# Optimization experiments

Hardware: AMD Instinct MI355X
Metric: run time of the kernel (lower is better)

Reference implementation:

```python
import jax, jax.numpy as jnp
import numpy as np

B, N, NG, K, H, C, BD = 4, 2048, 12, 16, 64, 128, 64
M = N // 4  # fps with down_sample=4
TWO_PI = 2.0 * np.pi


def _knn_idx(q, x, k):
    # q [Q,3] queries, x [P,3] pool -> [Q,k] indices of k nearest points in x
    d2 = jnp.sum((q[:, None, :] - x[None, :, :]) ** 2, axis=-1)
    _, idx = jax.lax.top_k(-d2, k)
    return idx


def _fps_idx(pos, m):
    # farthest point sampling, fixed m points, start at index 0
    n = pos.shape[0]
    def body(carry, _):
        d, last = carry
        dist = jnp.sum((pos - pos[last]) ** 2, axis=-1)
        d = jnp.minimum(d, dist)
        return (d, jnp.argmax(d)), last
    (_, _), idx = jax.lax.scan(body, (jnp.full((n,), 1e10, pos.dtype), jnp.int32(0)), None, length=m)
    return idx


def _basis_mlp(z, rff_w, w1, b1, w2, b2):
    # RFF -> Linear -> GELU -> Linear -> GELU
    p = TWO_PI * (z @ rff_w)
    f = jnp.concatenate([jnp.sin(p), jnp.cos(p)], axis=-1)
    h = jax.nn.gelu(f @ w1 + b1)
    return jax.nn.gelu(h @ w2 + b2)


def _interaction(x, nbr, kbx, kbR, kx_w, kx_b, kR_w, kR_b, mix_w, mix_b):
    # depthwise separable group conv: spatial gather-multiply-mean, then orientation mix
    kx = kbx @ kx_w + kx_b                     # [M,K,NG,C] spatial depthwise kernel
    kR = kbR @ kR_w + kR_b                     # [NG,NG,C] orientation depthwise kernel
    agg = jnp.mean(x[nbr] * kx, axis=1)        # [M,NG,C] mean over K neighbors
    y = jnp.einsum('bnc,mnc->bmc', agg, kR) / kR.shape[0]
    return x + jax.nn.gelu(y @ mix_w + mix_b)


def setup_inputs():
    key = jax.random.key(0)
    ks = iter(jax.random.split(key, 64))
    def randn(shape, std=1.0):
        return std * jax.random.normal(next(ks), shape, dtype=jnp.float32)
    inp = {}
    inp['pos'] = jax.random.uniform(next(ks), (B, N, 3), dtype=jnp.float32)
    nrm = randn((B, N, 3))
    inp['normal'] = nrm / jnp.linalg.norm(nrm, axis=-1, keepdims=True)
    g = randn((NG, 3))
    inp['grid'] = g / jnp.linalg.norm(g, axis=-1, keepdims=True)
    def lin(name, fin, fout):
        inp[name + '_w'] = randn((fin, fout), 1.0 / np.sqrt(fin))
        inp[name + '_b'] = jnp.zeros((fout,), jnp.float32)
    lin('emb1', 4, H); lin('emb2', H, H)
    lin('down', H, C)
    inp['bx_rff'] = randn((2, C // 2), 10.0)   # sigma=10
    lin('bx1', C, C); lin('bx2', C, BD)
    inp['bR_rff'] = randn((1, C // 2), 10.0)
    lin('bR1', C, C); lin('bR2', C, BD)
    for j in ('i1', 'i2'):
        lin(j + '_kx', BD, C); lin(j + '_kR', BD, C); lin(j + '_mix', C, C)
    lin('post1', C, 256); lin('post2', 256, 64); lin('post3', 64, 1)
    return inp


def reference(pos, normal, grid, emb1_w, emb1_b, emb2_w, emb2_b, down_w, down_b,
              bx_rff, bx1_w, bx1_b, bx2_w, bx2_b, bR_rff, bR1_w, bR1_b, bR2_w, bR2_b,
              i1_kx_w, i1_kx_b, i1_kR_w, i1_kR_b, i1_mix_w, i1_mix_b,
              i2_kx_w, i2_kx_b, i2_kR_w, i2_kR_b, i2_mix_w, i2_mix_b,
              post1_w, post1_b, post2_w, post2_b, post3_w, post3_b):
    def per_graph(p, nm):
        # lift: fiber features = <grid, normal> plus broadcast positions -> [N,NG,4]
        feat = jnp.concatenate([(nm @ grid.T)[:, :, None],
                                jnp.broadcast_to(p[:, None, :], (p.shape[0], NG, 3))], axis=-1)
        x = jax.nn.gelu(feat @ emb1_w + emb1_b) @ emb2_w + emb2_b   # [N,NG,H]
        # downsample block: fps + knn + linear/relu + scatter-max (exactly K edges per target)
        sel = _fps_idx(p, M)
        nbr_d = _knn_idx(p[sel], p, K)                               # [M,K] into N
        h = jax.nn.relu(x @ down_w + down_b)                         # [N,NG,C]
        x = jnp.max(h[nbr_d], axis=1)                                # [M,NG,C]
        ps = p[sel]
        # convolver block: knn graph + r3s2 edge attrs + basis MLPs + 2 interaction layers
        nbr = _knn_idx(ps, ps, K)                                    # [M,K] into M
        rel = ps[nbr] - ps[:, None, :]                               # pos[src]-pos[tgt], [M,K,3]
        rz = jnp.einsum('mke,ne->mkn', rel, grid)                    # [M,K,NG]
        rxy = jnp.sqrt(jnp.sum((rel[:, :, None, :] - rz[..., None] * grid) ** 2, axis=-1) + 1e-12)
        rpx = jnp.stack([rxy, rz], axis=-1)                          # [M,K,NG,2]
        rpR = (grid @ grid.T)[:, :, None]                            # [NG,NG,1]
        kbx = _basis_mlp(rpx, bx_rff, bx1_w, bx1_b, bx2_w, bx2_b)    # [M,K,NG,BD]
        kbR = _basis_mlp(rpR, bR_rff, bR1_w, bR1_b, bR2_w, bR2_b)    # [NG,NG,BD]
        x = _interaction(x, nbr, kbx, kbR, i1_kx_w, i1_kx_b, i1_kR_w, i1_kR_b, i1_mix_w, i1_mix_b)
        x = _interaction(x, nbr, kbx, kbR, i2_kx_w, i2_kx_b, i2_kR_w, i2_kR_b, i2_mix_w, i2_mix_b)
        # readout: mean over grid, global mean pool, MLP head
        g = jnp.mean(x, axis=(0, 1))                                 # [C]
        h1 = jax.nn.gelu(g @ post1_w + post1_b)
        h2 = jax.nn.gelu(h1 @ post2_w + post2_b)
        return h2 @ post3_w + post3_b                                # [1]
    return jax.vmap(per_graph)(pos, normal)                          # [B,1]
```

## Files before the change

kernel.cpp:

```cpp
#include <hip/hip_runtime.h>
#include <hip/hip_bf16.h>
#include <cfloat>

#define B_ 4
#define N_ 2048
#define NG_ 12
#define K_ 16
#define H_ 64
#define C_ 128
#define BD_ 64
#define M_ 512

typedef __attribute__((ext_vector_type(8))) short short8;
typedef __attribute__((ext_vector_type(4))) float floatx4;
typedef unsigned short ushort_t;
typedef unsigned int uint_t;

__device__ __forceinline__ float gelu_f(float x){
  float s = 0.7978845608028654f*(x + 0.044715f*x*x*x);
  float e = __expf(2.0f*s);
  float t = 1.0f - 2.0f/(e + 1.0f);
  return 0.5f*x*(1.0f + t);
}

__device__ __forceinline__ ushort_t bf16_rne(float x){
  uint_t u = __float_as_uint(x);
  uint_t r = (u + 0x7fffu + ((u >> 16) & 1u)) >> 16;
  return (ushort_t)r;
}

#define DPP_AMAX(CTRL) { \
  int _vb = __float_as_int(v); \
  int _ov = __builtin_amdgcn_update_dpp(_vb, _vb, (CTRL), 0xF, 0xF, false); \
  int _oi = __builtin_amdgcn_update_dpp(vi, vi, (CTRL), 0xF, 0xF, false); \
  float _of = __int_as_float(_ov); \
  bool _tk = (_of > v) || (_of == v && _oi < vi); \
  v = _tk ? _of : v; vi = _tk ? _oi : vi; }

#define DPP_AMIN(CTRL) { \
  int _vb = __float_as_int(v); \
  int _ov = __builtin_amdgcn_update_dpp(_vb, _vb, (CTRL), 0xF, 0xF, false); \
  int _oi = __builtin_amdgcn_update_dpp(vi, vi, (CTRL), 0xF, 0xF, false); \
  float _of = __int_as_float(_ov); \
  bool _tk = (_of < v) || (_of == v && _oi < vi); \
  v = _tk ? _of : v; vi = _tk ? _oi : vi; }

#define FPSB 4
#define LIFTB (B_*N_*NG_/4)
#define WSB 64
#define KBRB (NG_*NG_)

__global__ __launch_bounds__(256) void k_mega1(
    const float* __restrict__ pos, const float* __restrict__ normal,
    const float* __restrict__ grid,
    const float* __restrict__ e1w, const float* __restrict__ e1b,
    const float* __restrict__ e2w, const float* __restrict__ e2b,
    float* __restrict__ x1, float* __restrict__ ps,
    const float* __restrict__ bx1w, const float* __restrict__ bx2w,
    const float* __restrict__ kxw1, const float* __restrict__ kxw2,
    const float* __restrict__ dww,
    ushort_t* __restrict__ w1hiT, ushort_t* __restrict__ w1loT,
    ushort_t* __restrict__ w2hiT, ushort_t* __restrict__ w2loT,
    ushort_t* __restrict__ x1hiT, ushort_t* __restrict__ x1loT,
    ushort_t* __restrict__ x2hiT, ushort_t* __restrict__ x2loT,
    ushort_t* __restrict__ dwThi, ushort_t* __restrict__ dwTlo,
    const float* __restrict__ bR_rff,
    const float* __restrict__ bR1w, const float* __restrict__ bR1b,
    const float* __restrict__ bR2w, const float* __restrict__ bR2b,
    float* __restrict__ kbR){
  __shared__ float4 posS4[N_];
  __shared__ float2 wred[2][4];
  __shared__ float ts4[4][64];
  __shared__ float fsb[128], hsb[128];
  int bid = blockIdx.x;
  int tid = threadIdx.x;

  if (bid < FPSB){
    int b = bid;
    for (int i=tid;i<N_;i+=256){
      const float* p = pos + (size_t)b*N_*3 + (size_t)i*3;
      posS4[i] = make_float4(p[0], p[1], p[2], 0.f);
    }
    __syncthreads();
    float px[8],py[8],pz[8],d[8];
    #pragma unroll
    for (int j=0;j<8;++j){
      float4 pt = posS4[tid + 256*j];
      px[j]=pt.x; py[j]=pt.y; pz[j]=pt.z;
      d[j]=1e10f;
    }
    int wave = tid>>6, lane = tid&63;
    int last = 0;
    for (int s=0;s<M_;++s){
      float4 lp = posS4[last];
      float lx=lp.x, ly=lp.y, lz=lp.z;
      if (tid==0){ float* o = ps + ((size_t)b*M_+s)*3; o[0]=lx;o[1]=ly;o[2]=lz; }
      #pragma unroll
      for (int j=0;j<8;++j){
        float dx=__fsub_rn(px[j],lx), dy=__fsub_rn(py[j],ly), dz=__fsub_rn(pz[j],lz);
        float dist=__fadd_rn(__fadd_rn(__fmul_rn(dx,dx),__fmul_rn(dy,dy)),__fmul_rn(dz,dz));
        d[j]=fminf(d[j],dist);
      }
      if (s==M_-1) break;
      float va = d[1]>d[0]?d[1]:d[0]; int ja = d[1]>d[0]?1:0;
      float vb = d[3]>d[2]?d[3]:d[2]; int jb = d[3]>d[2]?3:2;
      float vc = d[5]>d[4]?d[5]:d[4]; int jc = d[5]>d[4]?5:4;
      float vd = d[7]>d[6]?d[7]:d[6]; int jd = d[7]>d[6]?7:6;
      float ve = vb>va?vb:va; int je = vb>va?jb:ja;
      float vf = vd>vc?vd:vc; int jf = vd>vc?jd:jc;
      float v  = vf>ve?vf:ve; int jj = vf>ve?jf:je;
      int vi = tid + (jj<<8);
      DPP_AMAX(0x121); DPP_AMAX(0x122); DPP_AMAX(0x124); DPP_AMAX(0x128);
      DPP_AMAX(0x142); DPP_AMAX(0x143);
      int sv = __builtin_amdgcn_readlane(__float_as_int(v), 63);
      int si = __builtin_amdgcn_readlane(vi, 63);
      if (lane==0) wred[s&1][wave] = make_float2(__int_as_float(sv), __int_as_float(si));
      __syncthreads();
      float2 r0 = wred[s&1][0], r1 = wred[s&1][1], r2 = wred[s&1][2], r3 = wred[s&1][3];
      float bv = r0.x; int bi = __float_as_int(r0.y);
      int i1 = __float_as_int(r1.y); if (r1.x>bv || (r1.x==bv && i1<bi)){ bv=r1.x; bi=i1; }
      int i2 = __float_as_int(r2.y); if (r2.x>bv || (r2.x==bv && i2<bi)){ bv=r2.x; bi=i2; }
      int i3 = __float_as_int(r3.y); if (r3.x>bv || (r3.x==bv && i3<bi)){ bv=r3.x; bi=i3; }
      last = bi;
    }
  } else if (bid < FPSB + LIFTB){
    int vbid = bid - FPSB;
    int q = tid>>6, lane = tid&63;
    int fid = vbid*4 + q;
    int g = fid % NG_;
    int n = (fid / NG_) % N_;
    int b = fid / (NG_*N_);
    const float* nm = normal + (size_t)(b*N_+n)*3;
    const float* pp = pos + (size_t)(b*N_+n)*3;
    const float* gg = grid + g*3;
    float f0 = nm[0]*gg[0] + nm[1]*gg[1] + nm[2]*gg[2];
    float t = e1b[lane] + f0*e1w[lane] + pp[0]*e1w[64+lane] + pp[1]*e1w[128+lane] + pp[2]*e1w[192+lane];
    ts4[q][lane] = gelu_f(t);
    __syncthreads();
    float acc = e2b[lane];
    #pragma unroll
    for (int i=0;i<64;++i) acc = fmaf(ts4[q][i], e2w[i*64+lane], acc);
    x1[(size_t)fid*64 + lane] = acc;
  } else if (bid < FPSB + LIFTB + WSB){
    int tg = (bid - FPSB - LIFTB)*256 + tid;
    if (tg < 16384){
      int j = tg >> 7, k = tg & 127;
      float x = bx1w[k*128 + j];
      ushort_t hi = bf16_rne(x);
      float hif = __uint_as_float(((uint_t)hi)<<16);
      ushort_t lo = bf16_rne(x - hif);
      w1hiT[tg] = hi; w1loT[tg] = lo;
    }
    if (tg < 8192){
      int c = tg >> 7, j = tg & 127;
      float x = bx2w[j*64 + c];
      ushort_t hi = bf16_rne(x);
      float hif = __uint_as_float(((uint_t)hi)<<16);
      ushort_t lo = bf16_rne(x - hif);
      w2hiT[tg] = hi; w2loT[tg] = lo;
    }
    if (tg < 8192){
      int c = tg >> 6, d = tg & 63;
      float xa = kxw1[d*128 + c];
      ushort_t hi = bf16_rne(xa);
      float hif = __uint_as_float(((uint_t)hi)<<16);
      ushort_t lo = bf16_rne(xa - hif);
      x1hiT[tg] = hi; x1loT[tg] = lo;
      float xb = kxw2[d*128 + c];
      ushort_t hi2 = bf16_rne(xb);
      float hif2 = __uint_as_float(((uint_t)hi2)<<16);
      ushort_t lo2 = bf16_rne(xb - hif2);
      x2hiT[tg] = hi2; x2loT[tg] = lo2;
      float xd = dww[d*128 + c];
      ushort_t hi3 = bf16_rne(xd);
      float hif3 = __uint_as_float(((uint_t)hi3)<<16);
      ushort_t lo3 = bf16_rne(xd - hif3);
      dwThi[tg] = hi3; dwTlo[tg] = lo3;
    }
  } else {
    int vbid = bid - FPSB - LIFTB - WSB;
    int gm = vbid / NG_, gn = vbid % NG_;
    int j = tid;
    if (j < 128){
      float z = grid[gm*3]*grid[gn*3] + grid[gm*3+1]*grid[gn*3+1] + grid[gm*3+2]*grid[gn*3+2];
      float ang = 6.283185307179586f * (z * bR_rff[j & 63]);
      fsb[j] = (j<64) ? sinf(ang) : cosf(ang);
    }
    __syncthreads();
    if (j < 128){
      float acc = bR1b[j];
      for (int i=0;i<128;++i) acc = fmaf(fsb[i], bR1w[i*128+j], acc);
      hsb[j] = gelu_f(acc);
    }
    __syncthreads();
    if (j < 64){
      float a2 = bR2b[j];
      for (int i=0;i<128;++i) a2 = fmaf(hsb[i], bR2w[i*64+j], a2);
      kbR[(size_t)vbid*64 + j] = gelu_f(a2);
    }
  }
}

template<int NP>
__device__ __forceinline__ void knn_body(int qm, const float* __restrict__ qp,
                                         const float* __restrict__ pool, int* __restrict__ out){
  constexpr int R = NP/64;
  int lane = threadIdx.x;
  int b = qm / M_;
  const float* q = qp + (size_t)qm*3;
  float qx=q[0], qy=q[1], qz=q[2];
  float d2[R];
  #pragma unroll
  for (int j=0;j<R;++j){
    int n = lane + 64*j;
    const float* p = pool + ((size_t)b*NP + n)*3;
    float dx=__fsub_rn(qx,p[0]), dy=__fsub_rn(qy,p[1]), dz=__fsub_rn(qz,p[2]);
    d2[j]=__fadd_rn(__fadd_rn(__fmul_rn(dx,dx),__fmul_rn(dy,dy)),__fmul_rn(dz,dz));
  }
  for (int r=0;r<K_;++r){
    float v=FLT_MAX; int vi=0x7fffffff;
    #pragma unroll
    for (int j=0;j<R;++j){
      if (d2[j]<v){ v=d2[j]; vi=lane+64*j; }
    }
    DPP_AMIN(0x121); DPP_AMIN(0x122); DPP_AMIN(0x124); DPP_AMIN(0x128);
    DPP_AMIN(0x142); DPP_AMIN(0x143);
    int si = __builtin_amdgcn_readlane(vi, 63);
    if (lane==0) out[(size_t)qm*K_ + r] = si;
    #pragma unroll
    for (int j=0;j<R;++j){ if (si == lane + 64*j) d2[j] = FLT_MAX; }
  }
}

__global__ __launch_bounds__(64) void k_knn_all(const float* __restrict__ psb,
    const float* __restrict__ pos, int* __restrict__ nbrD, int* __restrict__ nbrS){
  int bid = blockIdx.x;
  if (bid < B_*M_) knn_body<N_>(bid, psb, pos, nbrD);
  else             knn_body<M_>(bid - B_*M_, psb, psb, nbrS);
}

__global__ __launch_bounds__(128) void k_kR2(
    const float* __restrict__ kbR,
    const float* __restrict__ w1, const float* __restrict__ b1,
    const float* __restrict__ w2, const float* __restrict__ b2,
    float* __restrict__ o1, float* __restrict__ o2){
  int bid = blockIdx.x;
  int pair = bid % KBRB;
  const float* w = (bid < KBRB) ? w1 : w2;
  const float* bb = (bid < KBRB) ? b1 : b2;
  float* oo = (bid < KBRB) ? o1 : o2;
  int c = threadIdx.x;
  __shared__ float kb[64];
  if (c<64) kb[c] = kbR[(size_t)pair*64 + c];
  __syncthreads();
  float acc = bb[c];
  for (int d=0;d<64;++d) acc = fmaf(kb[d], w[d*128+c], acc);
  oo[(size_t)pair*128 + c] = acc;
}

__device__ __forceinline__ void dm_body(float* um, int bm,
    const float* __restrict__ x1, const int* __restrict__ nbrD,
    const ushort_t* __restrict__ dwThi, const ushort_t* __restrict__ dwTlo,
    const float* __restrict__ db, float* __restrict__ xA){
  int b = bm / M_;
  int tid = threadIdx.x;
  float* xs = um;
  int* nb = (int*)(um + 12288);
  if (tid < K_) nb[tid] = nbrD[(size_t)bm*K_ + tid];
  __syncthreads();
  for (int idx=tid; idx<3072; idx+=256){
    int k = idx / 192, qq = idx % 192;
    float4 vv = ((const float4*)&x1[((size_t)(b*N_) + nb[k])*(NG_*H_)])[qq];
    int gran = (qq >> 1) ^ (k & 7);
    *(float4*)&xs[k*768 + gran*8 + (qq&1)*4] = vv;
  }
  __syncthreads();
  int wid = tid>>6, lane = tid&63, ln = lane&15, g4 = lane>>4;
  short8 bh[2][2], bl[2][2];
  float dbv[2];
  #pragma unroll
  for (int nt=0; nt<2; ++nt){
    int col = wid*32 + nt*16 + ln;
    dbv[nt] = db[col];
    #pragma unroll
    for (int ks=0; ks<2; ++ks){
      bh[nt][ks] = *(const short8*)&dwThi[(size_t)col*64 + ks*32 + g4*8];
      bl[nt][ks] = *(const short8*)&dwTlo[(size_t)col*64 + ks*32 + g4*8];
    }
  }
  int xorl = ln & 7;
  #pragma unroll
  for (int g=0; g<NG_; ++g){
    short8 ah[2], al[2];
    #pragma unroll
    for (int ks=0; ks<2; ++ks){
      int col0 = g*64 + ks*32 + g4*8;
      int gran = (col0 >> 3) ^ xorl;
      const float* src = &xs[ln*768 + gran*8];
      float4 p0 = *(const float4*)src;
      float4 p1 = *(const float4*)(src+4);
      float hv[8] = {p0.x,p0.y,p0.z,p0.w,p1.x,p1.y,p1.z,p1.w};
      #pragma unroll
      for (int e=0; e<8; ++e){
        ushort_t hi = bf16_rne(hv[e]);
        float hif = __uint_as_float(((uint_t)hi)<<16);
        ushort_t lo = bf16_rne(hv[e]-hif);
        ah[ks][e] = (short)hi; al[ks][e] = (short)lo;
      }
    }
    floatx4 acc[2];
    acc[0] = (floatx4){0.f,0.f,0.f,0.f};
    acc[1] = (floatx4){0.f,0.f,0.f,0.f};
    #pragma unroll
    for (int nt=0; nt<2; ++nt)
      #pragma unroll
      for (int ks=0; ks<2; ++ks){
        acc[nt] = __builtin_amdgcn_mfma_f32_16x16x32_bf16(ah[ks], bh[nt][ks], acc[nt], 0,0,0);
        acc[nt] = __builtin_amdgcn_mfma_f32_16x16x32_bf16(al[ks], bh[nt][ks], acc[nt], 0,0,0);
        acc[nt] = __builtin_amdgcn_mfma_f32_16x16x32_bf16(ah[ks], bl[nt][ks], acc[nt], 0,0,0);
      }
    #pragma unroll
    for (int nt=0; nt<2; ++nt){
      float mx = fmaxf(fmaxf(acc[nt][0],acc[nt][1]), fmaxf(acc[nt][2],acc[nt][3]));
      mx = fmaxf(mx, __shfl_xor(mx, 16));
      mx = fmaxf(mx, __shfl_xor(mx, 32));
      if (g4 == 0)
        xA[(size_t)bm*(NG_*C_) + g*C_ + wid*32 + nt*16 + ln] = fmaxf(mx + dbv[nt], 0.0f);
    }
  }
}

__device__ __forceinline__ void kbx_body(float* um, int vbid,
    const float* __restrict__ ps, const int* __restrict__ nbr,
    const float* __restrict__ grid, const float* __restrict__ rff,
    const ushort_t* __restrict__ w1hiT, const ushort_t* __restrict__ w1loT,
    const ushort_t* __restrict__ w2hiT, const ushort_t* __restrict__ w2loT,
    const float* __restrict__ b1, const float* __restrict__ b2,
    float* __restrict__ kbx){
  float* z0s = um;
  float* z1s = um + 128;
  float* rws = um + 256;
  int tid = threadIdx.x;
  if (tid < 128){
    rws[tid] = rff[tid];
    int fid = vbid*128 + tid;
    int g = fid % NG_;
    int k = (fid/NG_) % K_;
    int bm = fid / (NG_*K_);
    int b = bm / M_;
    int nb = nbr[(size_t)bm*K_ + k];
    const float* pm = ps + (size_t)bm*3;
    const float* pn = ps + ((size_t)(b*M_) + nb)*3;
    float rx = pn[0]-pm[0], ry = pn[1]-pm[1], rz3 = pn[2]-pm[2];
    const float* gg = grid + g*3;
    float rz = rx*gg[0] + ry*gg[1] + rz3*gg[2];
    float vx = rx - rz*gg[0], vy = ry - rz*gg[1], vz = rz3 - rz*gg[2];
    float rxy = sqrtf(vx*vx + vy*vy + vz*vz + 1e-12f);
    z0s[tid]=rxy; z1s[tid]=rz;
  }
  __syncthreads();
  int wid = tid>>6, lane = tid&63;
  int ln = lane & 15, g = lane >> 4;
  float* bw = um + 384 + wid*1088;

  short8 ahi[2][4], alo[2][4];
  #pragma unroll
  for (int rt=0; rt<2; ++rt){
    float z0 = z0s[wid*32 + rt*16 + ln];
    float z1 = z1s[wid*32 + rt*16 + ln];
    #pragma unroll
    for (int ks=0; ks<4; ++ks){
      #pragma unroll
      for (int e=0; e<8; ++e){
        int kd = ks*32 + g*8 + e;
        int kk = kd & 63;
        float t = z0*rws[kk] + z1*rws[64+kk];
        t = t - floorf(t);
        float v = (ks < 2) ? __builtin_amdgcn_sinf(t) : __builtin_amdgcn_cosf(t);
        ushort_t hi = bf16_rne(v);
        float hif = __uint_as_float(((uint_t)hi)<<16);
        ushort_t lo = bf16_rne(v - hif);
        ahi[rt][ks][e] = (short)hi;
        alo[rt][ks][e] = (short)lo;
      }
    }
  }
  floatx4 acc2[2][4];
  #pragma unroll
  for (int rt=0; rt<2; ++rt)
    #pragma unroll
    for (int ct=0; ct<4; ++ct)
      acc2[rt][ct] = (floatx4){0.f,0.f,0.f,0.f};

  #pragma unroll
  for (int jp=0; jp<4; ++jp){
    floatx4 acc1[2][2];
    #pragma unroll
    for (int rt=0; rt<2; ++rt)
      #pragma unroll
      for (int jt=0; jt<2; ++jt)
        acc1[rt][jt] = (floatx4){0.f,0.f,0.f,0.f};
    #pragma unroll
    for (int ks=0; ks<4; ++ks){
      #pragma unroll
      for (int jt=0; jt<2; ++jt){
        int j = jp*32 + jt*16 + ln;
        short8 bhi = *(const short8*)&w1hiT[(size_t)j*128 + ks*32 + g*8];
        short8 blo = *(const short8*)&w1loT[(size_t)j*128 + ks*32 + g*8];
        #pragma unroll
        for (int rt=0; rt<2; ++rt){
          acc1[rt][jt] = __builtin_amdgcn_mfma_f32_16x16x32_bf16(ahi[rt][ks], bhi, acc1[rt][jt], 0,0,0);
          acc1[rt][jt] = __builtin_amdgcn_mfma_f32_16x16x32_bf16(alo[rt][ks], bhi, acc1[rt][jt], 0,0,0);
          acc1[rt][jt] = __builtin_amdgcn_mfma_f32_16x16x32_bf16(ahi[rt][ks], blo, acc1[rt][jt], 0,0,0);
        }
      }
    }
    #pragma unroll
    for (int jt=0; jt<2; ++jt){
      float bb = b1[jp*32 + jt*16 + ln];
      #pragma unroll
      for (int rt=0; rt<2; ++rt)
        #pragma unroll
        for (int i=0; i<4; ++i)
          bw[(rt*16 + g*4 + i)*34 + jt*16 + ln] = gelu_f(bb + acc1[rt][jt][i]);
    }
    #pragma unroll
    for (int rt=0; rt<2; ++rt){
      int base = (rt*16 + ln)*34 + g*8;
      float2 p0 = *(float2*)&bw[base+0];
      float2 p1 = *(float2*)&bw[base+2];
      float2 p2 = *(float2*)&bw[base+4];
      float2 p3 = *(float2*)&bw[base+6];
      float hv[8] = {p0.x,p0.y,p1.x,p1.y,p2.x,p2.y,p3.x,p3.y};
      short8 a2h, a2l;
      #pragma unroll
      for (int e=0; e<8; ++e){
        ushort_t hi = bf16_rne(hv[e]);
        float hif = __uint_as_float(((uint_t)hi)<<16);
        ushort_t lo = bf16_rne(hv[e] - hif);
        a2h[e] = (short)hi;
        a2l[e] = (short)lo;
      }
      #pragma unroll
      for (int ct=0; ct<4; ++ct){
        short8 b2h = *(const short8*)&w2hiT[(size_t)(ct*16+ln)*128 + jp*32 + g*8];
        short8 b2l = *(const short8*)&w2loT[(size_t)(ct*16+ln)*128 + jp*32 + g*8];
        acc2[rt][ct] = __builtin_amdgcn_mfma_f32_16x16x32_bf16(a2h, b2h, acc2[rt][ct], 0,0,0);
        acc2[rt][ct] = __builtin_amdgcn_mfma_f32_16x16x32_bf16(a2l, b2h, acc2[rt][ct], 0,0,0);
        acc2[rt][ct] = __builtin_amdgcn_mfma_f32_16x16x32_bf16(a2h, b2l, acc2[rt][ct], 0,0,0);
      }
    }
  }
  #pragma unroll
  for (int ct=0; ct<4; ++ct){
    float bb = b2[ct*16 + ln];
    #pragma unroll
    for (int rt=0; rt<2; ++rt)
      #pragma unroll
      for (int i=0; i<4; ++i){
        int row = wid*32 + rt*16 + g*4 + i;
        size_t fiber = (size_t)vbid*128 + row;
        kbx[fiber*64 + ct*16 + ln] = gelu_f(bb + acc2[rt][ct][i]);
      }
  }
}

__global__ __launch_bounds__(256) void k_dmkbx(
    const float* __restrict__ x1, const int* __restrict__ nbrD,
    const ushort_t* __restrict__ dwThi, const ushort_t* __restrict__ dwTlo,
    const float* __restrict__ db, float* __restrict__ xA,
    const float* __restrict__ ps, const int* __restrict__ nbrS,
    const float* __restrict__ grid, const float* __restrict__ rff,
    const ushort_t* __restrict__ w1hiT, const ushort_t* __restrict__ w1loT,
    const ushort_t* __restrict__ w2hiT, const ushort_t* __restrict__ w2loT,
    const float* __restrict__ b1, const float* __restrict__ b2,
    float* __restrict__ kbx){
  __shared__ __align__(16) float um[12384];
  int bid = blockIdx.x;
  if (bid < B_*M_)
    dm_body(um, bid, x1, nbrD, dwThi, dwTlo, db, xA);
  else
    kbx_body(um, bid - B_*M_, ps, nbrS, grid, rff, w1hiT, w1loT, w2hiT, w2loT, b1, b2, kbx);
}

__global__ __launch_bounds__(256) void k_inter(
    const float* __restrict__ xin, const int* __restrict__ nbr,
    const float* __restrict__ kbx, const float* __restrict__ kR,
    const ushort_t* __restrict__ kxhT, const ushort_t* __restrict__ kxlT,
    const float* __restrict__ kxb,
    const float* __restrict__ mw, const float* __restrict__ mb,
    float* __restrict__ xout){
  int bm = blockIdx.x; int b = bm / M_;
  int tid = threadIdx.x;
  int wid = tid>>6, lane = tid&63, ln = lane&15, g4 = lane>>4;
  int c = tid & 127, gh = tid >> 7;
  __shared__ float kbsL[48][68];
  __shared__ float Ts[48][130];
  __shared__ float aggS[NG_][C_];
  __shared__ float yS[NG_][C_];
  short8 bh[2][2], bl[2][2];
  float kxbv[2];
  #pragma unroll
  for (int nt=0; nt<2; ++nt){
    int cc_ = (wid*2+nt)*16 + ln;
    kxbv[nt] = kxb[cc_];
    #pragma unroll
    for (int ks=0; ks<2; ++ks){
      bh[nt][ks] = *(const short8*)&kxhT[(size_t)cc_*64 + ks*32 + g4*8];
      bl[nt][ks] = *(const short8*)&kxlT[(size_t)cc_*64 + ks*32 + g4*8];
    }
  }
  float accg[6] = {0,0,0,0,0,0};
  for (int cc=0; cc<4; ++cc){
    {
      const float4* src = (const float4*)(kbx + ((size_t)bm*192 + cc*48)*64);
      for (int idx=tid; idx<768; idx+=256){
        int r = idx >> 4, dq = idx & 15;
        *(float4*)&kbsL[r][dq*4] = src[idx];
      }
    }
    __syncthreads();
    floatx4 acc[3][2];
    #pragma unroll
    for (int mt=0; mt<3; ++mt)
      #pragma unroll
      for (int nt=0; nt<2; ++nt)
        acc[mt][nt] = (floatx4){0.f,0.f,0.f,0.f};
    #pragma unroll
    for (int mt=0; mt<3; ++mt){
      short8 ah[2], al[2];
      #pragma unroll
      for (int ks=0; ks<2; ++ks){
        float4 p0 = *(const float4*)&kbsL[mt*16+ln][ks*32+g4*8];
        float4 p1 = *(const float4*)&kbsL[mt*16+ln][ks*32+g4*8+4];
        float hv[8] = {p0.x,p0.y,p0.z,p0.w,p1.x,p1.y,p1.z,p1.w};
        #pragma unroll
        for (int e=0; e<8; ++e){
          ushort_t hi = bf16_rne(hv[e]);
          float hif = __uint_as_float(((uint_t)hi)<<16);
          ushort_t lo = bf16_rne(hv[e] - hif);
          ah[ks][e] = (short)hi;
          al[ks][e] = (short)lo;
        }
      }
      #pragma unroll
      for (int nt=0; nt<2; ++nt)
        #pragma unroll
        for (int ks=0; ks<2; ++ks){
          acc[mt][nt] = __builtin_amdgcn_mfma_f32_16x16x32_bf16(ah[ks], bh[nt][ks], acc[mt][nt], 0,0,0);
          acc[mt][nt] = __builtin_amdgcn_mfma_f32_16x16x32_bf16(al[ks], bh[nt][ks], acc[mt][nt], 0,0,0);
          acc[mt][nt] = __builtin_amdgcn_mfma_f32_16x16x32_bf16(ah[ks], bl[nt][ks], acc[mt][nt], 0,0,0);
        }
    }
    #pragma unroll
    for (int mt=0; mt<3; ++mt)
      #pragma unroll
      for (int nt=0; nt<2; ++nt)
        #pragma unroll
        for (int i=0; i<4; ++i)
          Ts[mt*16 + g4*4 + i][(wid*2+nt)*16 + ln] = acc[mt][nt][i] + kxbv[nt];
    __syncthreads();
    #pragma unroll
    for (int kl=0; kl<4; ++kl){
      int nb = nbr[(size_t)bm*K_ + cc*4 + kl];
      const float* xr = xin + ((size_t)(b*M_) + nb)*(NG_*C_);
      #pragma unroll
      for (int gi=0; gi<6; ++gi){
        int g = gh*6 + gi;
        accg[gi] = fmaf(Ts[kl*12+g][c], xr[g*C_ + c], accg[gi]);
      }
    }
    __syncthreads();
  }
  #pragma unroll
  for (int gi=0; gi<6; ++gi)
    aggS[gh*6+gi][c] = accg[gi] * (1.0f/16.0f);
  __syncthreads();
  #pragma unroll
  for (int gi=0; gi<6; ++gi){
    int g = gh*6+gi;
    float yv = 0.f;
    #pragma unroll
    for (int n=0;n<NG_;++n) yv = fmaf(aggS[n][c], kR[((size_t)g*NG_+n)*C_ + c], yv);
    yS[g][c] = yv * (1.0f/12.0f);
  }
  __syncthreads();
  float m6[6] = {0,0,0,0,0,0};
  for (int i4=0;i4<32;++i4){
    float w0 = mw[(i4*4+0)*C_+c], w1 = mw[(i4*4+1)*C_+c],
          w2 = mw[(i4*4+2)*C_+c], w3 = mw[(i4*4+3)*C_+c];
    #pragma unroll
    for (int gi=0;gi<6;++gi){
      int g = gh*6+gi;
      float4 yv = *(const float4*)&yS[g][i4*4];
      m6[gi] = fmaf(yv.x,w0,fmaf(yv.y,w1,fmaf(yv.z,w2,fmaf(yv.w,w3,m6[gi]))));
    }
  }
  float mbc = mb[c];
  #pragma unroll
  for (int gi=0;gi<6;++gi){
    int g = gh*6+gi;
    size_t off = (size_t)bm*(NG_*C_) + g*C_ + c;
    xout[off] = xin[off] + gelu_f(m6[gi] + mbc);
  }
}

__global__ __launch_bounds__(256) void k_reduce(
    const float* __restrict__ x, float* __restrict__ part){
  int blk = blockIdx.x;
  int b = blk >> 6, ch = blk & 63;
  int tid = threadIdx.x;
  int c = tid & 127, half = tid >> 7;
  const float* xb = x + (size_t)b*(M_*NG_)*C_;
  int r0 = ch*96;
  float acc = 0.f;
  for (int r = r0 + half; r < r0 + 96; r += 2)
    acc += xb[(size_t)r*C_ + c];
  __shared__ float red[256];
  red[tid] = acc;
  __syncthreads();
  if (half == 0)
    part[(size_t)blk*C_ + c] = red[c] + red[128 + c];
}

__global__ __launch_bounds__(256) void k_head(
    const float* __restrict__ part,
    const float* __restrict__ p1w, const float* __restrict__ p1b,
    const float* __restrict__ p2w, const float* __restrict__ p2b,
    const float* __restrict__ p3w, const float* __restrict__ p3b,
    float* __restrict__ out){
  int b = blockIdx.x, tid = threadIdx.x;
  __shared__ float gs[128];
  if (tid < 128){
    float a = 0.f;
    const float* pb = part + (size_t)b*64*C_;
    for (int ch = 0; ch < 64; ++ch) a += pb[(size_t)ch*C_ + tid];
    gs[tid] = a * (1.0f/(M_*NG_));
  }
  __syncthreads();
  __shared__ float h1[256];
  {
    float a = p1b[tid];
    for (int i=0;i<128;++i) a = fmaf(gs[i], p1w[i*256+tid], a);
    h1[tid] = gelu_f(a);
  }
  __syncthreads();
  __shared__ float h2[64];
  if (tid<64){
    float a = p2b[tid];
    for (int i=0;i<256;++i) a = fmaf(h1[i], p2w[i*64+tid], a);
    h2[tid] = gelu_f(a);
  }
  __syncthreads();
  if (tid==0){
    float a = p3b[0];
    for (int i=0;i<64;++i) a = fmaf(h2[i], p3w[i], a);
    out[b] = a;
  }
}

extern "C" void kernel_launch(void* const* d_in, const int* in_sizes, int n_in,
                              void* d_out, int out_size, void* d_ws, size_t ws_size,
                              hipStream_t stream){
  const float* pos    = (const float*)d_in[0];
  const float* normal = (const float*)d_in[1];
  const float* grid   = (const float*)d_in[2];
  const float* e1w = (const float*)d_in[3];  const float* e1b = (const float*)d_in[4];
  const float* e2w = (const float*)d_in[5];  const float* e2b = (const float*)d_in[6];
  const float* dww = (const float*)d_in[7];  const float* dwb = (const float*)d_in[8];
  const float* bx_rff = (const float*)d_in[9];
  const float* bx1w = (const float*)d_in[10]; const float* bx1b = (const float*)d_in[11];
  const float* bx2w = (const float*)d_in[12]; const float* bx2b = (const float*)d_in[13];
  const float* bR_rff = (const float*)d_in[14];
  const float* bR1w = (const float*)d_in[15]; const float* bR1b = (const float*)d_in[16];
  const float* bR2w = (const float*)d_in[17]; const float* bR2b = (const float*)d_in[18];
  const float* i1kxw = (const float*)d_in[19]; const float* i1kxb = (const float*)d_in[20];
  const float* i1kRw = (const float*)d_in[21]; const float* i1kRb = (const float*)d_in[22];
  const float* i1mw  = (const float*)d_in[23]; const float* i1mb  = (const float*)d_in[24];
  const float* i2kxw = (const float*)d_in[25]; const float* i2kxb = (const float*)d_in[26];
  const float* i2kRw = (const float*)d_in[27]; const float* i2kRb = (const float*)d_in[28];
  const float* i2mw  = (const float*)d_in[29]; const float* i2mb  = (const float*)d_in[30];
  const float* p1w = (const float*)d_in[31]; const float* p1b = (const float*)d_in[32];
  const float* p2w = (const float*)d_in[33]; const float* p2b = (const float*)d_in[34];
  const float* p3w = (const float*)d_in[35]; const float* p3b = (const float*)d_in[36];
  float* out = (float*)d_out;

  float* ws = (float*)d_ws;
  size_t o = 0;
  float* x1  = ws + o; o += (size_t)B_*N_*NG_*H_;
  float* psb = ws + o; o += (size_t)B_*M_*3;
  float* xA  = ws + o; o += (size_t)B_*M_*NG_*C_;
  float* xB  = ws + o; o += (size_t)B_*M_*NG_*C_;
  float* kbx = ws + o; o += (size_t)B_*M_*K_*NG_*BD_;
  float* kbR = ws + o; o += (size_t)NG_*NG_*BD_;
  float* kRb1 = ws + o; o += (size_t)NG_*NG_*C_;
  float* kRb2 = ws + o; o += (size_t)NG_*NG_*C_;
  float* part = ws + o; o += (size_t)B_*64*C_;
  int* nbrD  = (int*)(ws + o); o += (size_t)B_*M_*K_;
  int* nbrS  = (int*)(ws + o); o += (size_t)B_*M_*K_;
  ushort_t* w1hiT = (ushort_t*)(ws + o); o += 8192;
  ushort_t* w1loT = (ushort_t*)(ws + o); o += 8192;
  ushort_t* w2hiT = (ushort_t*)(ws + o); o += 4096;
  ushort_t* w2loT = (ushort_t*)(ws + o); o += 4096;
  ushort_t* x1hiT = (ushort_t*)(ws + o); o += 4096;
  ushort_t* x1loT = (ushort_t*)(ws + o); o += 4096;
  ushort_t* x2hiT = (ushort_t*)(ws + o); o += 4096;
  ushort_t* x2loT = (ushort_t*)(ws + o); o += 4096;
  ushort_t* dwThi = (ushort_t*)(ws + o); o += 4096;
  ushort_t* dwTlo = (ushort_t*)(ws + o); o += 4096;

  k_mega1<<<FPSB + LIFTB + WSB + KBRB, 256, 0, stream>>>(
      pos, normal, grid, e1w, e1b, e2w, e2b, x1, psb,
      bx1w, bx2w, i1kxw, i2kxw, dww,
      w1hiT, w1loT, w2hiT, w2loT, x1hiT, x1loT, x2hiT, x2loT, dwThi, dwTlo,
      bR_rff, bR1w, bR1b, bR2w, bR2b, kbR);
  k_knn_all<<<2*B_*M_, 64, 0, stream>>>(psb, pos, nbrD, nbrS);
  k_kR2<<<2*KBRB, 128, 0, stream>>>(kbR, i1kRw, i1kRb, i2kRw, i2kRb, kRb1, kRb2);
  k_dmkbx<<<B_*M_ + (B_*M_*K_*NG_)/128, 256, 0, stream>>>(
      x1, nbrD, dwThi, dwTlo, dwb, xA,
      psb, nbrS, grid, bx_rff, w1hiT, w1loT, w2hiT, w2loT, bx1b, bx2b, kbx);
  k_inter<<<B_*M_, 256, 0, stream>>>(xA, nbrS, kbx, kRb1, x1hiT, x1loT, i1kxb, i1mw, i1mb, xB);
  k_inter<<<B_*M_, 256, 0, stream>>>(xB, nbrS, kbx, kRb2, x2hiT, x2loT, i2kxb, i2mw, i2mb, xA);
  k_reduce<<<B_*64, 256, 0, stream>>>(xA, part);
  k_head<<<B_, 256, 0, stream>>>(part, p1w, p1b, p2w, p2b, p3w, p3b, out);
}
```

Before: 802.8 us.

## Pre-split activations to packed bf16 hi/lo, fuse kR projection and pooling reduction

x1 and kbx are now stored as packed bf16 hi/lo pairs at production time, so the consumers (dm_body and k_inter, where kbx is read twice) unpack them with byte permutes instead of redoing the split-rounding on every load. The kR projection kernel is folded into the kbR block of k_mega1, and the global mean-pool reduction moves into the epilogue of the second k_inter with per-row partials, which drops two launches. In exchange, k_head now sums 512 partial rows per batch instead of 64.

```diff
diff --git a/kernel.cpp b/kernel.cpp
--- a/kernel.cpp
+++ b/kernel.cpp
@@ -29,6 +29,23 @@
   return (ushort_t)r;
 }
 
+__device__ __forceinline__ uint_t pack_hl(float x){
+  ushort_t hi = bf16_rne(x);
+  float hif = __uint_as_float(((uint_t)hi)<<16);
+  ushort_t lo = bf16_rne(x - hif);
+  return (uint_t)hi | ((uint_t)lo << 16);
+}
+
+__device__ __forceinline__ uint_t perm_lo16(uint_t a, uint_t b){ return __builtin_amdgcn_perm(a, b, 0x05040100u); }
+__device__ __forceinline__ uint_t perm_hi16(uint_t a, uint_t b){ return __builtin_amdgcn_perm(a, b, 0x07060302u); }
+
+#define UNPACK8(Q0, Q1, AH, AL) { \
+  uint_t* _ap = (uint_t*)&(AH); uint_t* _lp = (uint_t*)&(AL); \
+  _ap[0] = perm_lo16((Q0).y, (Q0).x); _ap[1] = perm_lo16((Q0).w, (Q0).z); \
+  _ap[2] = perm_lo16((Q1).y, (Q1).x); _ap[3] = perm_lo16((Q1).w, (Q1).z); \
+  _lp[0] = perm_hi16((Q0).y, (Q0).x); _lp[1] = perm_hi16((Q0).w, (Q0).z); \
+  _lp[2] = perm_hi16((Q1).y, (Q1).x); _lp[3] = perm_hi16((Q1).w, (Q1).z); }
+
 #define DPP_AMAX(CTRL) { \
   int _vb = __float_as_int(v); \
   int _ov = __builtin_amdgcn_update_dpp(_vb, _vb, (CTRL), 0xF, 0xF, false); \
@@ -55,7 +72,7 @@
     const float* __restrict__ grid,
     const float* __restrict__ e1w, const float* __restrict__ e1b,
     const float* __restrict__ e2w, const float* __restrict__ e2b,
-    float* __restrict__ x1, float* __restrict__ ps,
+    uint_t* __restrict__ x1p, float* __restrict__ ps,
     const float* __restrict__ bx1w, const float* __restrict__ bx2w,
     const float* __restrict__ kxw1, const float* __restrict__ kxw2,
     const float* __restrict__ dww,
@@ -67,7 +84,9 @@
     const float* __restrict__ bR_rff,
     const float* __restrict__ bR1w, const float* __restrict__ bR1b,
     const float* __restrict__ bR2w, const float* __restrict__ bR2b,
-    float* __restrict__ kbR){
+    const float* __restrict__ kR1w, const float* __restrict__ kR1b,
+    const float* __restrict__ kR2w, const float* __restrict__ kR2b,
+    float* __restrict__ kRb1, float* __restrict__ kRb2){
   __shared__ float4 posS4[N_];
   __shared__ float2 wred[2][4];
   __shared__ float ts4[4][64];
@@ -140,7 +159,7 @@
     float acc = e2b[lane];
     #pragma unroll
     for (int i=0;i<64;++i) acc = fmaf(ts4[q][i], e2w[i*64+lane], acc);
-    x1[(size_t)fid*64 + lane] = acc;
+    x1p[(size_t)fid*64 + lane] = pack_hl(acc);
   } else if (bid < FPSB + LIFTB + WSB){
     int tg = (bid - FPSB - LIFTB)*256 + tid;
     if (tg < 16384){
@@ -196,7 +215,18 @@
     if (j < 64){
       float a2 = bR2b[j];
       for (int i=0;i<128;++i) a2 = fmaf(hsb[i], bR2w[i*64+j], a2);
-      kbR[(size_t)vbid*64 + j] = gelu_f(a2);
+      fsb[j] = gelu_f(a2);
+    }
+    __syncthreads();
+    if (j < 128){
+      float a1 = kR1b[j], a2v = kR2b[j];
+      for (int d=0; d<64; ++d){
+        float kv = fsb[d];
+        a1  = fmaf(kv, kR1w[d*128+j], a1);
+        a2v = fmaf(kv, kR2w[d*128+j], a2v);
+      }
+      kRb1[(size_t)vbid*128 + j] = a1;
+      kRb2[(size_t)vbid*128 + j] = a2v;
     }
   }
 }
@@ -239,40 +269,21 @@
   else             knn_body<M_>(bid - B_*M_, psb, psb, nbrS);
 }
 
-__global__ __launch_bounds__(128) void k_kR2(
-    const float* __restrict__ kbR,
-    const float* __restrict__ w1, const float* __restrict__ b1,
-    const float* __restrict__ w2, const float* __restrict__ b2,
-    float* __restrict__ o1, float* __restrict__ o2){
-  int bid = blockIdx.x;
-  int pair = bid % KBRB;
-  const float* w = (bid < KBRB) ? w1 : w2;
-  const float* bb = (bid < KBRB) ? b1 : b2;
-  float* oo = (bid < KBRB) ? o1 : o2;
-  int c = threadIdx.x;
-  __shared__ float kb[64];
-  if (c<64) kb[c] = kbR[(size_t)pair*64 + c];
-  __syncthreads();
-  float acc = bb[c];
-  for (int d=0;d<64;++d) acc = fmaf(kb[d], w[d*128+c], acc);
-  oo[(size_t)pair*128 + c] = acc;
-}
-
-__device__ __forceinline__ void dm_body(float* um, int bm,
-    const float* __restrict__ x1, const int* __restrict__ nbrD,
+__device__ __forceinline__ void dm_body(uint_t* um, int bm,
+    const uint_t* __restrict__ x1p, const int* __restrict__ nbrD,
     const ushort_t* __restrict__ dwThi, const ushort_t* __restrict__ dwTlo,
     const float* __restrict__ db, float* __restrict__ xA){
   int b = bm / M_;
   int tid = threadIdx.x;
-  float* xs = um;
+  uint_t* xs = um;
   int* nb = (int*)(um + 12288);
   if (tid < K_) nb[tid] = nbrD[(size_t)bm*K_ + tid];
   __syncthreads();
   for (int idx=tid; idx<3072; idx+=256){
     int k = idx / 192, qq = idx % 192;
-    float4 vv = ((const float4*)&x1[((size_t)(b*N_) + nb[k])*(NG_*H_)])[qq];
+    uint4 vv = ((const uint4*)&x1p[((size_t)(b*N_) + nb[k])*(NG_*H_)])[qq];
     int gran = (qq >> 1) ^ (k & 7);
-    *(float4*)&xs[k*768 + gran*8 + (qq&1)*4] = vv;
+    *(uint4*)&xs[k*768 + gran*8 + (qq&1)*4] = vv;
   }
   __syncthreads();
   int wid = tid>>6, lane = tid&63, ln = lane&15, g4 = lane>>4;
@@ -296,17 +307,10 @@
     for (int ks=0; ks<2; ++ks){
       int col0 = g*64 + ks*32 + g4*8;
       int gran = (col0 >> 3) ^ xorl;
-      const float* src = &xs[ln*768 + gran*8];
-      float4 p0 = *(const float4*)src;
-      float4 p1 = *(const float4*)(src+4);
-      float hv[8] = {p0.x,p0.y,p0.z,p0.w,p1.x,p1.y,p1.z,p1.w};
-      #pragma unroll
-      for (int e=0; e<8; ++e){
-        ushort_t hi = bf16_rne(hv[e]);
-        float hif = __uint_as_float(((uint_t)hi)<<16);
-        ushort_t lo = bf16_rne(hv[e]-hif);
-        ah[ks][e] = (short)hi; al[ks][e] = (short)lo;
-      }
+      const uint_t* src = &xs[ln*768 + gran*8];
+      uint4 q0 = *(const uint4*)src;
+      uint4 q1 = *(const uint4*)(src+4);
+      UNPACK8(q0, q1, ah[ks], al[ks]);
     }
     floatx4 acc[2];
     acc[0] = (floatx4){0.f,0.f,0.f,0.f};
@@ -336,7 +340,7 @@
     const ushort_t* __restrict__ w1hiT, const ushort_t* __restrict__ w1loT,
     const ushort_t* __restrict__ w2hiT, const ushort_t* __restrict__ w2loT,
     const float* __restrict__ b1, const float* __restrict__ b2,
-    float* __restrict__ kbx){
+    uint_t* __restrict__ kbxp){
   float* z0s = um;
   float* z1s = um + 128;
   float* rws = um + 256;
@@ -460,13 +464,13 @@
       for (int i=0; i<4; ++i){
         int row = wid*32 + rt*16 + g*4 + i;
         size_t fiber = (size_t)vbid*128 + row;
-        kbx[fiber*64 + ct*16 + ln] = gelu_f(bb + acc2[rt][ct][i]);
+        kbxp[fiber*64 + ct*16 + ln] = pack_hl(gelu_f(bb + acc2[rt][ct][i]));
       }
   }
 }
 
 __global__ __launch_bounds__(256) void k_dmkbx(
-    const float* __restrict__ x1, const int* __restrict__ nbrD,
+    const uint_t* __restrict__ x1p, const int* __restrict__ nbrD,
     const ushort_t* __restrict__ dwThi, const ushort_t* __restrict__ dwTlo,
     const float* __restrict__ db, float* __restrict__ xA,
     const float* __restrict__ ps, const int* __restrict__ nbrS,
@@ -474,30 +478,31 @@
     const ushort_t* __restrict__ w1hiT, const ushort_t* __restrict__ w1loT,
     const ushort_t* __restrict__ w2hiT, const ushort_t* __restrict__ w2loT,
     const float* __restrict__ b1, const float* __restrict__ b2,
-    float* __restrict__ kbx){
-  __shared__ __align__(16) float um[12384];
+    uint_t* __restrict__ kbxp){
+  __shared__ __align__(16) uint_t um[12384];
   int bid = blockIdx.x;
   if (bid < B_*M_)
-    dm_body(um, bid, x1, nbrD, dwThi, dwTlo, db, xA);
+    dm_body(um, bid, x1p, nbrD, dwThi, dwTlo, db, xA);
   else
-    kbx_body(um, bid - B_*M_, ps, nbrS, grid, rff, w1hiT, w1loT, w2hiT, w2loT, b1, b2, kbx);
+    kbx_body((float*)um, bid - B_*M_, ps, nbrS, grid, rff, w1hiT, w1loT, w2hiT, w2loT, b1, b2, kbxp);
 }
 
 __global__ __launch_bounds__(256) void k_inter(
     const float* __restrict__ xin, const int* __restrict__ nbr,
-    const float* __restrict__ kbx, const float* __restrict__ kR,
+    const uint_t* __restrict__ kbxp, const float* __restrict__ kR,
     const ushort_t* __restrict__ kxhT, const ushort_t* __restrict__ kxlT,
     const float* __restrict__ kxb,
     const float* __restrict__ mw, const float* __restrict__ mb,
-    float* __restrict__ xout){
+    float* __restrict__ xout, float* __restrict__ part){
   int bm = blockIdx.x; int b = bm / M_;
   int tid = threadIdx.x;
   int wid = tid>>6, lane = tid&63, ln = lane&15, g4 = lane>>4;
   int c = tid & 127, gh = tid >> 7;
-  __shared__ float kbsL[48][68];
+  __shared__ uint_t kbsL[48][68];
   __shared__ float Ts[48][130];
   __shared__ float aggS[NG_][C_];
   __shared__ float yS[NG_][C_];
+  __shared__ float psumS[2][C_];
   short8 bh[2][2], bl[2][2];
   float kxbv[2];
   #pragma unroll
@@ -513,10 +518,10 @@
   float accg[6] = {0,0,0,0,0,0};
   for (int cc=0; cc<4; ++cc){
     {
-      const float4* src = (const float4*)(kbx + ((size_t)bm*192 + cc*48)*64);
+      const uint4* src = (const uint4*)(kbxp + ((size_t)bm*192 + cc*48)*64);
       for (int idx=tid; idx<768; idx+=256){
         int r = idx >> 4, dq = idx & 15;
-        *(float4*)&kbsL[r][dq*4] = src[idx];
+        *(uint4*)&kbsL[r][dq*4] = src[idx];
       }
     }
     __syncthreads();
@@ -531,17 +536,10 @@
       short8 ah[2], al[2];
       #pragma unroll
       for (int ks=0; ks<2; ++ks){
-        float4 p0 = *(const float4*)&kbsL[mt*16+ln][ks*32+g4*8];
-        float4 p1 = *(const float4*)&kbsL[mt*16+ln][ks*32+g4*8+4];
-        float hv[8] = {p0.x,p0.y,p0.z,p0.w,p1.x,p1.y,p1.z,p1.w};
-        #pragma unroll
-        for (int e=0; e<8; ++e){
-          ushort_t hi = bf16_rne(hv[e]);
-          float hif = __uint_as_float(((uint_t)hi)<<16);
-          ushort_t lo = bf16_rne(hv[e] - hif);
-          ah[ks][e] = (short)hi;
-          al[ks][e] = (short)lo;
-        }
+        const uint_t* src = &kbsL[mt*16+ln][ks*32+g4*8];
+        uint4 q0 = *(const uint4*)src;
+        uint4 q1 = *(const uint4*)(src+4);
+        UNPACK8(q0, q1, ah[ks], al[ks]);
       }
       #pragma unroll
       for (int nt=0; nt<2; ++nt)
@@ -597,30 +595,21 @@
     }
   }
   float mbc = mb[c];
+  float psum = 0.f;
   #pragma unroll
   for (int gi=0;gi<6;++gi){
     int g = gh*6+gi;
     size_t off = (size_t)bm*(NG_*C_) + g*C_ + c;
-    xout[off] = xin[off] + gelu_f(m6[gi] + mbc);
-  }
-}
-
-__global__ __launch_bounds__(256) void k_reduce(
-    const float* __restrict__ x, float* __restrict__ part){
-  int blk = blockIdx.x;
-  int b = blk >> 6, ch = blk & 63;
-  int tid = threadIdx.x;
-  int c = tid & 127, half = tid >> 7;
-  const float* xb = x + (size_t)b*(M_*NG_)*C_;
-  int r0 = ch*96;
-  float acc = 0.f;
-  for (int r = r0 + half; r < r0 + 96; r += 2)
-    acc += xb[(size_t)r*C_ + c];
-  __shared__ float red[256];
-  red[tid] = acc;
-  __syncthreads();
-  if (half == 0)
-    part[(size_t)blk*C_ + c] = red[c] + red[128 + c];
+    float val = xin[off] + gelu_f(m6[gi] + mbc);
+    xout[off] = val;
+    psum += val;
+  }
+  if (part){
+    psumS[gh][c] = psum;
+    __syncthreads();
+    if (gh == 0)
+      part[(size_t)bm*C_ + c] = psumS[0][c] + psumS[1][c];
+  }
 }
 
 __global__ __launch_bounds__(256) void k_head(
@@ -630,13 +619,22 @@
     const float* __restrict__ p3w, const float* __restrict__ p3b,
     float* __restrict__ out){
   int b = blockIdx.x, tid = threadIdx.x;
+  int c = tid & 127, half = tid >> 7;
+  __shared__ float red[256];
   __shared__ float gs[128];
-  if (tid < 128){
-    float a = 0.f;
-    const float* pb = part + (size_t)b*64*C_;
-    for (int ch = 0; ch < 64; ++ch) a += pb[(size_t)ch*C_ + tid];
-    gs[tid] = a * (1.0f/(M_*NG_));
-  }
+  {
+    const float* pb = part + (size_t)b*M_*C_;
+    float a0=0.f,a1=0.f,a2=0.f,a3=0.f;
+    for (int r = half*4; r < M_; r += 8){
+      a0 += pb[(size_t)(r+0)*C_ + c];
+      a1 += pb[(size_t)(r+1)*C_ + c];
+      a2 += pb[(size_t)(r+2)*C_ + c];
+      a3 += pb[(size_t)(r+3)*C_ + c];
+    }
+    red[tid] = (a0+a1)+(a2+a3);
+  }
+  __syncthreads();
+  if (half==0) gs[c] = (red[c] + red[128+c]) * (1.0f/(M_*NG_));
   __syncthreads();
   __shared__ float h1[256];
   {
@@ -687,15 +685,14 @@
 
   float* ws = (float*)d_ws;
   size_t o = 0;
-  float* x1  = ws + o; o += (size_t)B_*N_*NG_*H_;
+  uint_t* x1p = (uint_t*)(ws + o); o += (size_t)B_*N_*NG_*H_;
   float* psb = ws + o; o += (size_t)B_*M_*3;
   float* xA  = ws + o; o += (size_t)B_*M_*NG_*C_;
   float* xB  = ws + o; o += (size_t)B_*M_*NG_*C_;
-  float* kbx = ws + o; o += (size_t)B_*M_*K_*NG_*BD_;
-  float* kbR = ws + o; o += (size_t)NG_*NG_*BD_;
+  uint_t* kbxp = (uint_t*)(ws + o); o += (size_t)B_*M_*K_*NG_*BD_;
   float* kRb1 = ws + o; o += (size_t)NG_*NG_*C_;
   float* kRb2 = ws + o; o += (size_t)NG_*NG_*C_;
-  float* part = ws + o; o += (size_t)B_*64*C_;
+  float* part = ws + o; o += (size_t)B_*M_*C_;
   int* nbrD  = (int*)(ws + o); o += (size_t)B_*M_*K_;
   int* nbrS  = (int*)(ws + o); o += (size_t)B_*M_*K_;
   ushort_t* w1hiT = (ushort_t*)(ws + o); o += 8192;
@@ -710,17 +707,16 @@
   ushort_t* dwTlo = (ushort_t*)(ws + o); o += 4096;
 
   k_mega1<<<FPSB + LIFTB + WSB + KBRB, 256, 0, stream>>>(
-      pos, normal, grid, e1w, e1b, e2w, e2b, x1, psb,
+      pos, normal, grid, e1w, e1b, e2w, e2b, x1p, psb,
       bx1w, bx2w, i1kxw, i2kxw, dww,
       w1hiT, w1loT, w2hiT, w2loT, x1hiT, x1loT, x2hiT, x2loT, dwThi, dwTlo,
-      bR_rff, bR1w, bR1b, bR2w, bR2b, kbR);
+      bR_rff, bR1w, bR1b, bR2w, bR2b,
+      i1kRw, i1kRb, i2kRw, i2kRb, kRb1, kRb2);
   k_knn_all<<<2*B_*M_, 64, 0, stream>>>(psb, pos, nbrD, nbrS);
-  k_kR2<<<2*KBRB, 128, 0, stream>>>(kbR, i1kRw, i1kRb, i2kRw, i2kRb, kRb1, kRb2);
   k_dmkbx<<<B_*M_ + (B_*M_*K_*NG_)/128, 256, 0, stream>>>(
-      x1, nbrD, dwThi, dwTlo, dwb, xA,
-      psb, nbrS, grid, bx_rff, w1hiT, w1loT, w2hiT, w2loT, bx1b, bx2b, kbx);
-  k_inter<<<B_*M_, 256, 0, stream>>>(xA, nbrS, kbx, kRb1, x1hiT, x1loT, i1kxb, i1mw, i1mb, xB);
-  k_inter<<<B_*M_, 256, 0, stream>>>(xB, nbrS, kbx, kRb2, x2hiT, x2loT, i2kxb, i2mw, i2mb, xA);
-  k_reduce<<<B_*64, 256, 0, stream>>>(xA, part);
+      x1p, nbrD, dwThi, dwTlo, dwb, xA,
+      psb, nbrS, grid, bx_rff, w1hiT, w1loT, w2hiT, w2loT, bx1b, bx2b, kbxp);
+  k_inter<<<B_*M_, 256, 0, stream>>>(xA, nbrS, kbxp, kRb1, x1hiT, x1loT, i1kxb, i1mw, i1mb, xB, nullptr);
+  k_inter<<<B_*M_, 256, 0, stream>>>(xB, nbrS, kbxp, kRb2, x2hiT, x2loT, i2kxb, i2mw, i2mb, xA, part);
   k_head<<<B_, 256, 0, stream>>>(part, p1w, p1b, p2w, p2b, p3w, p3b, out);
 }
```

Result: no change. 793.7 us (-1.1%).
